# Kernel tuning notes

Hardware: AMD Instinct MI355X
Metric: run time of the kernel (lower is better)

Reference implementation:

```python
import jax, jax.numpy as jnp
import numpy as np

TEMP = 0.07
WEIGHT = 0.5
EPS = 1e-8  # matches torch F.cosine_similarity norm clamp


def setup_inputs() -> dict:
    key = jax.random.key(0)
    k1, k2, k3 = jax.random.split(key, 3)
    B, T, D = 64, 512, 512
    video = jax.random.normal(k1, (B, T, D), dtype=jnp.float32)
    audio = jax.random.normal(k2, (B, T, D), dtype=jnp.float32)
    mask = jax.random.randint(k3, (B, T), 0, 2, dtype=jnp.int32)
    return {"video": video, "audio": audio, "mask": mask}


def reference(video, audio, mask):
    B, T, D = video.shape
    # L2-normalize features (cosine similarity = dot of normalized vectors)
    vn = video / jnp.clip(jnp.linalg.norm(video, axis=-1, keepdims=True), EPS)
    an = audio / jnp.clip(jnp.linalg.norm(audio, axis=-1, keepdims=True), EPS)
    idx = jnp.argmax(mask, axis=1)                                   # [B]
    a_anchor = jnp.take_along_axis(an, idx[:, None, None], axis=1)[:, 0]  # [B,D]
    v_anchor = jnp.take_along_axis(vn, idx[:, None, None], axis=1)[:, 0]  # [B,D]
    # scaled cosine sims of all timesteps vs the anchor of the other modality
    sims_a2v = jnp.einsum('btd,bd->bt', vn, a_anchor) / TEMP         # cos(v_j, a_idx)/T
    sims_v2a = jnp.einsum('btd,bd->bt', an, v_anchor) / TEMP         # cos(a_j, v_idx)/T
    # positive: cos(v_idx, a_idx)/T (same for both directions)
    pos = jnp.take_along_axis(sims_a2v, idx[:, None], axis=1)[:, 0]  # [B]
    not_pos = jnp.arange(T)[None, :] != idx[:, None]                 # [B,T]
    neg_a = jnp.sum(jnp.where(not_pos, jnp.exp(sims_a2v), 0.0), axis=1)  # a2v negatives
    neg_v = jnp.sum(jnp.where(not_pos, jnp.exp(sims_v2a), 0.0), axis=1)  # v2a negatives
    pos_exp = jnp.exp(pos)
    batch_loss_a = jnp.sum(-jnp.log(pos_exp / neg_a))
    batch_loss_v = jnp.sum(-jnp.log(pos_exp / neg_v))
    return ((batch_loss_a * WEIGHT + batch_loss_v * WEIGHT) / B).reshape(1)
```

## Files before the change

### kernel.cpp

```cpp
#include <hip/hip_runtime.h>
#include <math.h>

#define TEMP_INV (1.0f / 0.07f)
#define WEIGHT 0.5f
#define EPS 1e-8f
#define BB 64
#define TT 512
#define DD 512
#define RR 8

__device__ inline float wave_sum(float v) {
    for (int o = 32; o >= 1; o >>= 1) v += __shfl_xor(v, o, 64);
    return v;
}
__device__ inline int wave_max_i(int v) {
    for (int o = 32; o >= 1; o >>= 1) v = max(v, __shfl_xor(v, o, 64));
    return v;
}
__device__ inline int wave_min_i(int v) {
    for (int o = 32; o >= 1; o >>= 1) v = min(v, __shfl_xor(v, o, 64));
    return v;
}

__global__ __launch_bounds__(256) void prep_kernel(
    const float* __restrict__ video, const float* __restrict__ audio,
    const int* __restrict__ mask,
    float* __restrict__ a_anchor, float* __restrict__ v_anchor,
    float* __restrict__ pos, float* __restrict__ neg, int* __restrict__ idx_out)
{
    const int b = blockIdx.x;
    const int tid = threadIdx.x;
    const int wid = tid >> 6, lane = tid & 63;
    __shared__ int sh_i[4];
    __shared__ float sh_f[4][3];
    __shared__ int s_idx;
    __shared__ float s_inva, s_invv;

    int m0 = mask[b * TT + tid];
    int m1 = mask[b * TT + tid + 256];
    int vmax = wave_max_i(max(m0, m1));
    if (lane == 0) sh_i[wid] = vmax;
    __syncthreads();
    if (tid == 0) {
        int r = sh_i[0];
        for (int i = 1; i < 4; i++) r = max(r, sh_i[i]);
        sh_i[0] = r;
    }
    __syncthreads();
    vmax = sh_i[0];
    __syncthreads();
    int cand = (m0 == vmax) ? tid : 0x7fffffff;
    int cand1 = (m1 == vmax) ? (tid + 256) : 0x7fffffff;
    cand = min(cand, cand1);
    cand = wave_min_i(cand);
    if (lane == 0) sh_i[wid] = cand;
    __syncthreads();
    if (tid == 0) {
        int r = sh_i[0];
        for (int i = 1; i < 4; i++) r = min(r, sh_i[i]);
        s_idx = r;
    }
    __syncthreads();
    const int idx = s_idx;

    const float* arow = audio + ((size_t)(b * TT + idx)) * DD;
    const float* vrow = video + ((size_t)(b * TT + idx)) * DD;
    float a0 = arow[tid], a1 = arow[tid + 256];
    float v0 = vrow[tid], v1 = vrow[tid + 256];
    float ssa = a0 * a0 + a1 * a1;
    float ssv = v0 * v0 + v1 * v1;
    float dav = a0 * v0 + a1 * v1;
    ssa = wave_sum(ssa);
    ssv = wave_sum(ssv);
    dav = wave_sum(dav);
    if (lane == 0) { sh_f[wid][0] = ssa; sh_f[wid][1] = ssv; sh_f[wid][2] = dav; }
    __syncthreads();
    if (tid == 0) {
        float ra = 0.f, rv = 0.f, rd = 0.f;
        for (int i = 0; i < 4; i++) { ra += sh_f[i][0]; rv += sh_f[i][1]; rd += sh_f[i][2]; }
        float inva = 1.0f / fmaxf(sqrtf(ra), EPS);
        float invv = 1.0f / fmaxf(sqrtf(rv), EPS);
        s_inva = inva; s_invv = invv;
        pos[b] = rd * inva * invv * TEMP_INV;
        neg[b] = 0.0f;
        neg[BB + b] = 0.0f;
        idx_out[b] = idx;
    }
    __syncthreads();
    const float inva = s_inva, invv = s_invv;
    a_anchor[b * DD + tid] = a0 * inva;
    a_anchor[b * DD + tid + 256] = a1 * inva;
    v_anchor[b * DD + tid] = v0 * invv;
    v_anchor[b * DD + tid + 256] = v1 * invv;
}

__global__ __launch_bounds__(256) void sims_kernel(
    const float* __restrict__ video, const float* __restrict__ audio,
    const float* __restrict__ a_anchor, const float* __restrict__ v_anchor,
    const int* __restrict__ idx_arr, float* __restrict__ neg)
{
    const int b = blockIdx.y;
    const int dir = blockIdx.z;
    const int wid = threadIdx.x >> 6, lane = threadIdx.x & 63;
    const int t0 = blockIdx.x * (4 * RR) + wid * RR;

    const float* base = (dir == 0 ? video : audio) + (size_t)b * TT * DD;
    const float* anc = (dir == 0 ? a_anchor : v_anchor) + b * DD;

    float4 c0 = *(const float4*)(anc + lane * 4);
    float4 c1 = *(const float4*)(anc + 256 + lane * 4);

    float4 r0[RR], r1[RR];
#pragma unroll
    for (int r = 0; r < RR; r++) {
        const float* row = base + (size_t)(t0 + r) * DD;
        r0[r] = *(const float4*)(row + lane * 4);
        r1[r] = *(const float4*)(row + 256 + lane * 4);
    }

    float dot[RR], nrm[RR];
#pragma unroll
    for (int r = 0; r < RR; r++) {
        dot[r] = r0[r].x * c0.x + r0[r].y * c0.y + r0[r].z * c0.z + r0[r].w * c0.w
               + r1[r].x * c1.x + r1[r].y * c1.y + r1[r].z * c1.z + r1[r].w * c1.w;
        nrm[r] = r0[r].x * r0[r].x + r0[r].y * r0[r].y + r0[r].z * r0[r].z + r0[r].w * r0[r].w
               + r1[r].x * r1[r].x + r1[r].y * r1[r].y + r1[r].z * r1[r].z + r1[r].w * r1[r].w;
    }

#pragma unroll
    for (int o = 32; o >= 1; o >>= 1) {
#pragma unroll
        for (int r = 0; r < RR; r++) {
            dot[r] += __shfl_xor(dot[r], o, 64);
            nrm[r] += __shfl_xor(nrm[r], o, 64);
        }
    }

    if (lane == 0) {
        const int idx = idx_arr[b];
        float local = 0.0f;
#pragma unroll
        for (int r = 0; r < RR; r++) {
            const int t = t0 + r;
            float sim = dot[r] / fmaxf(sqrtf(nrm[r]), EPS) * TEMP_INV;
            local += (t == idx) ? 0.0f : expf(sim);
        }
        atomicAdd(&neg[dir * BB + b], local);
    }
}

__global__ void finalize_kernel(const float* __restrict__ pos,
                                const float* __restrict__ neg,
                                float* __restrict__ out)
{
    const int b = threadIdx.x;
    float term = WEIGHT * (logf(neg[b]) + logf(neg[BB + b])) - pos[b];
    term = wave_sum(term);
    if (b == 0) out[0] = term / (float)BB;
}

extern "C" void kernel_launch(void* const* d_in, const int* in_sizes, int n_in,
                              void* d_out, int out_size, void* d_ws, size_t ws_size,
                              hipStream_t stream)
{
    const float* video = (const float*)d_in[0];
    const float* audio = (const float*)d_in[1];
    const int* mask = (const int*)d_in[2];

    float* ws = (float*)d_ws;
    float* a_anchor = ws;
    float* v_anchor = ws + BB * DD;
    float* pos = ws + 2 * BB * DD;
    float* neg = pos + BB;
    int* idx = (int*)(neg + 2 * BB);

    prep_kernel<<<BB, 256, 0, stream>>>(video, audio, mask, a_anchor, v_anchor, pos, neg, idx);
    dim3 grid(TT / (4 * RR), BB, 2);
    sims_kernel<<<grid, 256, 0, stream>>>(video, audio, a_anchor, v_anchor, idx, neg);
    finalize_kernel<<<1, 64, 0, stream>>>(pos, neg, (float*)d_out);
}
```

Baseline: 167.6 us.

## Stage sims rows through LDS with direct global-to-LDS loads, smaller blocks

```diff
diff --git a/kernel.cpp b/kernel.cpp
--- a/kernel.cpp
+++ b/kernel.cpp
@@ -7,7 +7,12 @@
 #define BB 64
 #define TT 512
 #define DD 512
-#define RR 8
+#define ROWS_PER_BLOCK 16
+
+#define GLOAD_LDS(gp, lp)                                              \
+    __builtin_amdgcn_global_load_lds(                                  \
+        (const __attribute__((address_space(1))) void*)(gp),           \
+        (__attribute__((address_space(3))) void*)(lp), 16, 0, 0)
 
 __device__ inline float wave_sum(float v) {
     for (int o = 32; o >= 1; o >>= 1) v += __shfl_xor(v, o, 64);
@@ -101,36 +106,42 @@
 {
     const int b = blockIdx.y;
     const int dir = blockIdx.z;
-    const int wid = threadIdx.x >> 6, lane = threadIdx.x & 63;
-    const int t0 = blockIdx.x * (4 * RR) + wid * RR;
+    const int tid = threadIdx.x;
+    const int wid = tid >> 6, lane = tid & 63;
+    const int t0 = blockIdx.x * ROWS_PER_BLOCK;
 
-    const float* base = (dir == 0 ? video : audio) + (size_t)b * TT * DD;
-    const float* anc = (dir == 0 ? a_anchor : v_anchor) + b * DD;
+    __shared__ float lds[ROWS_PER_BLOCK * DD];
 
-    float4 c0 = *(const float4*)(anc + lane * 4);
-    float4 c1 = *(const float4*)(anc + 256 + lane * 4);
+    const float* base = (dir == 0 ? video : audio)
+                      + (size_t)b * TT * DD + (size_t)t0 * DD;
 
-    float4 r0[RR], r1[RR];
 #pragma unroll
-    for (int r = 0; r < RR; r++) {
-        const float* row = base + (size_t)(t0 + r) * DD;
-        r0[r] = *(const float4*)(row + lane * 4);
-        r1[r] = *(const float4*)(row + 256 + lane * 4);
+    for (int i = 0; i < 8; i++) {
+        GLOAD_LDS(base + (i * 256 + tid) * 4, &lds[(i * 256 + tid) * 4]);
     }
 
-    float dot[RR], nrm[RR];
+    const float* anc = (dir == 0 ? a_anchor : v_anchor) + b * DD;
+    float4 c0 = *(const float4*)(anc + lane * 8);
+    float4 c1 = *(const float4*)(anc + lane * 8 + 4);
+
+    __syncthreads();
+
+    float dot[4], nrm[4];
 #pragma unroll
-    for (int r = 0; r < RR; r++) {
-        dot[r] = r0[r].x * c0.x + r0[r].y * c0.y + r0[r].z * c0.z + r0[r].w * c0.w
-               + r1[r].x * c1.x + r1[r].y * c1.y + r1[r].z * c1.z + r1[r].w * c1.w;
-        nrm[r] = r0[r].x * r0[r].x + r0[r].y * r0[r].y + r0[r].z * r0[r].z + r0[r].w * r0[r].w
-               + r1[r].x * r1[r].x + r1[r].y * r1[r].y + r1[r].z * r1[r].z + r1[r].w * r1[r].w;
+    for (int r = 0; r < 4; r++) {
+        const float* row = &lds[(wid * 4 + r) * DD];
+        float4 x0 = *(const float4*)(row + lane * 8);
+        float4 x1 = *(const float4*)(row + lane * 8 + 4);
+        dot[r] = x0.x * c0.x + x0.y * c0.y + x0.z * c0.z + x0.w * c0.w
+               + x1.x * c1.x + x1.y * c1.y + x1.z * c1.z + x1.w * c1.w;
+        nrm[r] = x0.x * x0.x + x0.y * x0.y + x0.z * x0.z + x0.w * x0.w
+               + x1.x * x1.x + x1.y * x1.y + x1.z * x1.z + x1.w * x1.w;
     }
 
 #pragma unroll
     for (int o = 32; o >= 1; o >>= 1) {
 #pragma unroll
-        for (int r = 0; r < RR; r++) {
+        for (int r = 0; r < 4; r++) {
             dot[r] += __shfl_xor(dot[r], o, 64);
             nrm[r] += __shfl_xor(nrm[r], o, 64);
         }
@@ -140,8 +151,8 @@
         const int idx = idx_arr[b];
         float local = 0.0f;
 #pragma unroll
-        for (int r = 0; r < RR; r++) {
-            const int t = t0 + r;
+        for (int r = 0; r < 4; r++) {
+            const int t = t0 + wid * 4 + r;
             float sim = dot[r] / fmaxf(sqrtf(nrm[r]), EPS) * TEMP_INV;
             local += (t == idx) ? 0.0f : expf(sim);
         }
@@ -175,7 +186,7 @@
     int* idx = (int*)(neg + 2 * BB);
 
     prep_kernel<<<BB, 256, 0, stream>>>(video, audio, mask, a_anchor, v_anchor, pos, neg, idx);
-    dim3 grid(TT / (4 * RR), BB, 2);
+    dim3 grid(TT / ROWS_PER_BLOCK, BB, 2);
     sims_kernel<<<grid, 256, 0, stream>>>(video, audio, a_anchor, v_anchor, idx, neg);
     finalize_kernel<<<1, 64, 0, stream>>>(pos, neg, (float*)d_out);
 }
```

After: 208.3 us. +24.3%, slower.
